# Kernel tuning notes

Hardware: AMD Instinct MI355X
Metric: run time of the kernel (lower is better)

## Reference

```python
import jax, jax.numpy as jnp
import numpy as np

B, L, D_IN, H = 16, 2048, 1024, 512  # bidirectional: out_size = 2*H = D_IN (k=3 SRU layout)


def setup_inputs() -> dict:
    key = jax.random.key(0)
    k1, k2, k3, k4 = jax.random.split(key, 4)
    x = jax.random.normal(k1, (B, L, D_IN), dtype=jnp.float32)
    W = jax.random.normal(k2, (D_IN, 2, H, 3), dtype=jnp.float32) * 0.02
    bf = jax.random.normal(k3, (2, H), dtype=jnp.float32) * 0.02
    br = jax.random.normal(k4, (2, H), dtype=jnp.float32) * 0.02
    return {"x": x, "W": W, "bf": bf, "br": br}


def _sru_scan(xtil, f, r, xres, reverse):
    # xtil/f/r/xres: (L, B, H). Diagonal linear recurrence:
    #   c_t = f_t * c_{t-1} + (1 - f_t) * xtil_t
    #   h_t = r_t * tanh(c_t) + (1 - r_t) * xres_t
    def step(c, inp):
        xt_, f_, r_, xr_ = inp
        c = f_ * c + (1.0 - f_) * xt_
        h = r_ * jnp.tanh(c) + (1.0 - r_) * xr_
        return c, h
    c0 = jnp.zeros(xtil.shape[1:], dtype=xtil.dtype)
    c_last, h = jax.lax.scan(step, c0, (xtil, f, r, xres), reverse=reverse)
    return h, c_last


def reference(x, W, bf, br):
    xt = jnp.transpose(x, (1, 0, 2))  # (L, B, D_IN), as the wrapper does x.transpose(0,1)
    # U: (L, B, 2 dirs, H, 3 = [x_tilde, f_pre, r_pre])
    U = jnp.einsum("lbi,idhk->lbdhk", xt, W)
    f = jax.nn.sigmoid(U[..., 1] + bf[None, None, :, :])  # (L,B,2,H)
    r = jax.nn.sigmoid(U[..., 2] + br[None, None, :, :])
    xtil = U[..., 0]
    # highway/residual: raw input split per direction since n_in == 2*H (k=3)
    xres = xt.reshape(L, B, 2, H)

    h_f, c_f = _sru_scan(xtil[:, :, 0], f[:, :, 0], r[:, :, 0], xres[:, :, 0], reverse=False)
    h_b, c_b = _sru_scan(xtil[:, :, 1], f[:, :, 1], r[:, :, 1], xres[:, :, 1], reverse=True)

    h = jnp.concatenate([h_f, h_b], axis=-1)          # (L, B, 2H)
    c = jnp.concatenate([c_f, c_b], axis=-1)          # (B, 2H) final cell states
    # wrapper returns (out.transpose(0,1), c.transpose(0,1))
    return jnp.transpose(h, (1, 0, 2)), c.T
```

## Files before the change

kernel.cpp:

```cpp
#include <hip/hip_runtime.h>
#include <stdint.h>

#define B_    16
#define L_    2048
#define DIN_  1024
#define H_    512
#define NCOL_ 3072
#define M_    (B_ * L_)
#define K_    DIN_
#define NCHUNK 16
#define CHUNK  128

typedef unsigned short u16;
typedef __bf16 bf16_t;
typedef bf16_t bf16x8 __attribute__((ext_vector_type(8)));
typedef float  f32x4  __attribute__((ext_vector_type(4)));

__device__ __forceinline__ u16 f2bf(float f) {
  union { float f; uint32_t u; } v; v.f = f;
  return (u16)((v.u + 0x7fffu + ((v.u >> 16) & 1u)) >> 16);
}
__device__ __forceinline__ float bf2f(u16 b) {
  union { uint32_t u; float f; } v; v.u = ((uint32_t)b) << 16; return v.f;
}
__device__ __forceinline__ u16 f2h(float f) {
  _Float16 h = (_Float16)f; return *(u16*)&h;
}
__device__ __forceinline__ float h2f(u16 b) {
  _Float16 h = *(_Float16*)&b; return (float)h;
}

__global__ void cvt_x_kernel(const float4* __restrict__ x, ushort4* __restrict__ xb) {
  int i = blockIdx.x * blockDim.x + threadIdx.x;
  float4 v = x[i];
  ushort4 o;
  o.x = f2bf(v.x); o.y = f2bf(v.y); o.z = f2bf(v.z); o.w = f2bf(v.w);
  xb[i] = o;
}

__global__ void transpose_w_kernel(const float* __restrict__ W, u16* __restrict__ Wt) {
  __shared__ float s[32][33];
  int n0 = blockIdx.x * 32;
  int i0 = blockIdx.y * 32;
  int tx = threadIdx.x, ty = threadIdx.y;
  #pragma unroll
  for (int y = 0; y < 32; y += 8)
    s[ty + y][tx] = W[(uint64_t)(i0 + ty + y) * NCOL_ + n0 + tx];
  __syncthreads();
  #pragma unroll
  for (int y = 0; y < 32; y += 8) {
    int n = n0 + ty + y;
    int kk = n % 3, d = n / 1536, h = (n % 1536) / 3;
    int np = kk * 1024 + d * 512 + h;
    Wt[(uint64_t)np * K_ + i0 + tx] = f2bf(s[tx][ty + y]);
  }
}

__device__ __forceinline__ void gload_lds16(const void* g, void* lds) {
  __builtin_amdgcn_global_load_lds(
      (const __attribute__((address_space(1))) uint32_t*)g,
      (__attribute__((address_space(3))) uint32_t*)lds, 16, 0, 0);
}

__device__ __forceinline__ bf16x8 lds_rd(const u16* lds, int byteOff) {
  return __builtin_bit_cast(bf16x8, *(const f32x4*)((const char*)lds + byteOff));
}

__global__ __launch_bounds__(512, 2) void gemm_u_kernel(const u16* __restrict__ A,
                                                        const u16* __restrict__ Bt,
                                                        const float* __restrict__ bfp,
                                                        const float* __restrict__ brp,
                                                        u16* __restrict__ xtilP,
                                                        u16* __restrict__ fP,
                                                        u16* __restrict__ rP) {
  __shared__ __align__(16) u16 lds[81920];

  const int bid = blockIdx.x;
  const int xcd = bid & 7;
  const int li  = bid >> 3;
  const int bm  = xcd * 16 + (li & 15);
  const int bn  = li >> 4;
  const int m0 = bm * 256, n0 = bn * 256;

  const int tid  = threadIdx.x;
  const int w    = tid >> 6, lane = tid & 63;
  const int wr   = w >> 2, wc = w & 3;
  const int rr   = lane & 15, hs = lane >> 4;
  const int swzRd = (rr & 7) << 4;
  const int hsOff = hs * 16;

  const int rStage = w * 8 + (lane >> 3);
  const int sCol   = ((lane & 7) ^ ((lane >> 3) & 7)) * 8;
  const int ldsChunk = w * 1024;

  f32x4 acc[8][4] = {};

  auto stageA = [&](int bufBase, int kt) {
    #pragma unroll
    for (int h = 0; h < 2; ++h)
      #pragma unroll
      for (int j = 0; j < 2; ++j)
        gload_lds16(A + (uint64_t)(m0 + h * 128 + j * 64 + rStage) * K_ + kt + sCol,
                    (char*)lds + bufBase + h * 16384 + j * 8192 + ldsChunk);
  };
  auto stageB = [&](int bufBase, int kt) {
    #pragma unroll
    for (int h = 0; h < 2; ++h)
      #pragma unroll
      for (int j = 0; j < 2; ++j)
        gload_lds16(Bt + (uint64_t)(n0 + h * 128 + j * 64 + rStage) * K_ + kt + sCol,
                    (char*)lds + bufBase + h * 16384 + j * 8192 + ldsChunk);
  };

  stageA(0, 0);
  stageB(65536, 0);
  stageB(65536 + 32768, 64);
  asm volatile("s_waitcnt vmcnt(4)" ::: "memory");
  __builtin_amdgcn_sched_barrier(0);
  __builtin_amdgcn_s_barrier();

  const int aHalfBase = wr * 16384;
  const int bQuart    = (wc >> 1) * 16384;
  const int rowB0     = (wc & 1) * 64;

  int b3 = 0;
  for (int t = 0; t < 16; ++t) {
    const int curA = (t & 1) << 15;
    const int curB = 65536 + b3 * 32768;
    const int b3n2 = (b3 >= 1) ? (b3 - 1) : 2;

    if (t < 15) stageA((~t & 1) << 15, (t + 1) * 64);
    bf16x8 aF[4][2], bF[4][2];
    #pragma unroll
    for (int a = 0; a < 4; ++a)
      #pragma unroll
      for (int ks = 0; ks < 2; ++ks)
        aF[a][ks] = lds_rd(lds, curA + aHalfBase + (a * 16 + rr) * 128 + ((ks * 64 + hsOff) ^ swzRd));
    #pragma unroll
    for (int ni = 0; ni < 4; ++ni)
      #pragma unroll
      for (int ks = 0; ks < 2; ++ks)
        bF[ni][ks] = lds_rd(lds, curB + bQuart + (rowB0 + ni * 16 + rr) * 128 + ((ks * 64 + hsOff) ^ swzRd));
    __builtin_amdgcn_sched_barrier(0);
    __builtin_amdgcn_s_barrier();
    asm volatile("s_waitcnt lgkmcnt(0)" ::: "memory");
    __builtin_amdgcn_sched_barrier(0);
    __builtin_amdgcn_s_setprio(1);
    #pragma unroll
    for (int a = 0; a < 4; ++a)
      #pragma unroll
      for (int ni = 0; ni < 4; ++ni)
        #pragma unroll
        for (int ks = 0; ks < 2; ++ks)
          acc[a][ni] = __builtin_amdgcn_mfma_f32_16x16x32_bf16(aF[a][ks], bF[ni][ks], acc[a][ni], 0, 0, 0);
    __builtin_amdgcn_s_setprio(0);
    __builtin_amdgcn_sched_barrier(0);
    __builtin_amdgcn_s_barrier();

    if (t < 14) stageB(65536 + b3n2 * 32768, (t + 2) * 64);
    bf16x8 aG[4][2];
    #pragma unroll
    for (int a = 0; a < 4; ++a)
      #pragma unroll
      for (int ks = 0; ks < 2; ++ks)
        aG[a][ks] = lds_rd(lds, curA + aHalfBase + ((a + 4) * 16 + rr) * 128 + ((ks * 64 + hsOff) ^ swzRd));
    __builtin_amdgcn_sched_barrier(0);
    __builtin_amdgcn_s_barrier();
    asm volatile("s_waitcnt lgkmcnt(0)" ::: "memory");
    __builtin_amdgcn_sched_barrier(0);
    __builtin_amdgcn_s_setprio(1);
    #pragma unroll
    for (int a = 0; a < 4; ++a)
      #pragma unroll
      for (int ni = 0; ni < 4; ++ni)
        #pragma unroll
        for (int ks = 0; ks < 2; ++ks)
          acc[a + 4][ni] = __builtin_amdgcn_mfma_f32_16x16x32_bf16(aG[a][ks], bF[ni][ks], acc[a + 4][ni], 0, 0, 0);
    __builtin_amdgcn_s_setprio(0);
    if (t < 14) {
      asm volatile("s_waitcnt vmcnt(4)" ::: "memory");
      __builtin_amdgcn_sched_barrier(0);
    } else if (t == 14) {
      asm volatile("s_waitcnt vmcnt(0)" ::: "memory");
      __builtin_amdgcn_sched_barrier(0);
    }
    __builtin_amdgcn_s_barrier();

    b3 = (b3 + 1 == 3) ? 0 : b3 + 1;
  }

  const int kkPlane = n0 >> 10;
  const int chBase  = n0 & 1023;
  u16* plane = (kkPlane == 0) ? xtilP : (kkPlane == 1 ? fP : rP);
  const float* biasp = (kkPlane == 1) ? bfp : brp;
  #pragma unroll
  for (int mi = 0; mi < 8; ++mi) {
    #pragma unroll
    for (int ni = 0; ni < 4; ++ni) {
      const int ch = chBase + wc * 64 + ni * 16 + rr;
      const float bias = kkPlane ? biasp[ch] : 0.f;
      #pragma unroll
      for (int i = 0; i < 4; ++i) {
        const int row = m0 + wr * 128 + mi * 16 + hs * 4 + i;
        float v = acc[mi][ni][i];
        if (kkPlane) v = 1.f / (1.f + __expf(-(v + bias)));
        plane[(uint64_t)row * 1024 + ch] = f2h(v);
      }
    }
  }
}

__global__ __launch_bounds__(256) void scan_partial_kernel(const u16* __restrict__ xtilP,
                                                           const u16* __restrict__ fP,
                                                           float* __restrict__ cpart,
                                                           float* __restrict__ Pp) {
  int tid = blockIdx.x * 256 + threadIdx.x;
  int ch = tid & 1023, chunk = (tid >> 10) & (NCHUNK - 1), b = tid >> 14;
  int d = ch >> 9;
  int l = chunk * CHUNK + (d ? CHUNK - 1 : 0);
  int64_t stride = d ? -1024 : 1024;
  uint64_t base = ((uint64_t)b * L_ + l) * 1024 + ch;
  float c = 0.f, P = 1.f;
  #pragma unroll 4
  for (int it = 0; it < CHUNK; ++it) {
    float f  = h2f(fP[base]);
    float xt = h2f(xtilP[base]);
    c = f * c + (1.f - f) * xt;
    P *= f;
    base += stride;
  }
  int o = (b * NCHUNK + chunk) * 1024 + ch;
  cpart[o] = c;
  Pp[o] = P;
}

__global__ void scan_combine_kernel(const float* __restrict__ cpart, const float* __restrict__ Pp,
                                    float* __restrict__ cin, float* __restrict__ outc) {
  int tid = blockIdx.x * blockDim.x + threadIdx.x;
  int ch = tid & 1023, b = tid >> 10, d = ch >> 9;
  float c = 0.f;
  for (int i = 0; i < NCHUNK; ++i) {
    int chunk = d ? (NCHUNK - 1 - i) : i;
    int o = (b * NCHUNK + chunk) * 1024 + ch;
    cin[o] = c;
    c = cpart[o] + Pp[o] * c;
  }
  outc[ch * B_ + b] = c;
}

__global__ __launch_bounds__(256) void scan_final_kernel(const u16* __restrict__ xb,
                                                         const u16* __restrict__ xtilP,
                                                         const u16* __restrict__ fP,
                                                         const u16* __restrict__ rP,
                                                         const float* __restrict__ cin,
                                                         float* __restrict__ outh) {
  int tid = blockIdx.x * 256 + threadIdx.x;
  int ch = tid & 1023, chunk = (tid >> 10) & (NCHUNK - 1), b = tid >> 14;
  int d = ch >> 9;
  int l = chunk * CHUNK + (d ? CHUNK - 1 : 0);
  int64_t stride = d ? -1024 : 1024;
  uint64_t base = ((uint64_t)b * L_ + l) * 1024 + ch;
  float c = cin[(b * NCHUNK + chunk) * 1024 + ch];
  #pragma unroll 2
  for (int it = 0; it < CHUNK; ++it) {
    float f    = h2f(fP[base]);
    float xt   = h2f(xtilP[base]);
    float rr   = h2f(rP[base]);
    float xres = bf2f(xb[base]);
    c = f * c + (1.f - f) * xt;
    float th = 1.f - 2.f / (__expf(2.f * c) + 1.f);
    outh[base] = rr * th + (1.f - rr) * xres;
    base += stride;
  }
}

extern "C" void kernel_launch(void* const* d_in, const int* in_sizes, int n_in,
                              void* d_out, int out_size, void* d_ws, size_t ws_size,
                              hipStream_t stream) {
  const float* x   = (const float*)d_in[0];
  const float* W   = (const float*)d_in[1];
  const float* bfp = (const float*)d_in[2];
  const float* brp = (const float*)d_in[3];

  float* outh = (float*)d_out;
  float* outc = outh + (size_t)B_ * L_ * DIN_;

  u16* xb = (u16*)d_ws;
  u16* Wt = xb + (size_t)M_ * K_;
  u16* xtilP = Wt + (size_t)NCOL_ * K_;
  u16* fP    = xtilP + (size_t)M_ * 1024;
  u16* rP    = fP    + (size_t)M_ * 1024;
  float* cpart = (float*)Wt;
  float* Pp    = cpart + (size_t)B_ * NCHUNK * 1024;
  float* cin   = Pp    + (size_t)B_ * NCHUNK * 1024;

  cvt_x_kernel<<<(M_ * K_ / 4) / 256, 256, 0, stream>>>((const float4*)x, (ushort4*)xb);
  transpose_w_kernel<<<dim3(NCOL_ / 32, K_ / 32), dim3(32, 8), 0, stream>>>(W, Wt);
  gemm_u_kernel<<<(M_ / 256) * (NCOL_ / 256), 512, 0, stream>>>(xb, Wt, bfp, brp, xtilP, fP, rP);
  scan_partial_kernel<<<(B_ * NCHUNK * 1024) / 256, 256, 0, stream>>>(xtilP, fP, cpart, Pp);
  scan_combine_kernel<<<(B_ * 2 * H_) / 256, 256, 0, stream>>>(cpart, Pp, cin, outc);
  scan_final_kernel<<<(B_ * NCHUNK * 1024) / 256, 256, 0, stream>>>(xb, xtilP, fP, rP, cin, outh);
}
```

Baseline: 384.6 us.

## Collapse GEMM k-loop to single barrier and interleave A fragment loads with MFMAs

The main GEMM loop drops its two mid-iteration barriers and explicit lgkmcnt waits, issuing both the A and B global-to-LDS stages at the top of each iteration. A-fragment reads are split into four pairs of row blocks, each interleaved with its MFMAs, so LDS reads can overlap matrix math and fewer registers are live at once. The loop is marked unroll 1, and the final iteration skips its trailing barrier. The aim is less synchronization and better overlap, but the code relies on the compiler's own waitcnt placement and loses the setprio hints. Safety rests on the existing triple-buffered B and double-buffered A schedule.

```diff
diff --git a/kernel.cpp b/kernel.cpp
--- a/kernel.cpp
+++ b/kernel.cpp
@@ -124,59 +124,39 @@
   const int rowB0     = (wc & 1) * 64;
 
   int b3 = 0;
+  #pragma unroll 1
   for (int t = 0; t < 16; ++t) {
     const int curA = (t & 1) << 15;
     const int curB = 65536 + b3 * 32768;
     const int b3n2 = (b3 >= 1) ? (b3 - 1) : 2;
 
     if (t < 15) stageA((~t & 1) << 15, (t + 1) * 64);
-    bf16x8 aF[4][2], bF[4][2];
-    #pragma unroll
-    for (int a = 0; a < 4; ++a)
-      #pragma unroll
-      for (int ks = 0; ks < 2; ++ks)
-        aF[a][ks] = lds_rd(lds, curA + aHalfBase + (a * 16 + rr) * 128 + ((ks * 64 + hsOff) ^ swzRd));
+    if (t < 14) stageB(65536 + b3n2 * 32768, (t + 2) * 64);
+
+    bf16x8 bF[4][2];
     #pragma unroll
     for (int ni = 0; ni < 4; ++ni)
       #pragma unroll
       for (int ks = 0; ks < 2; ++ks)
         bF[ni][ks] = lds_rd(lds, curB + bQuart + (rowB0 + ni * 16 + rr) * 128 + ((ks * 64 + hsOff) ^ swzRd));
-    __builtin_amdgcn_sched_barrier(0);
-    __builtin_amdgcn_s_barrier();
-    asm volatile("s_waitcnt lgkmcnt(0)" ::: "memory");
-    __builtin_amdgcn_sched_barrier(0);
-    __builtin_amdgcn_s_setprio(1);
-    #pragma unroll
-    for (int a = 0; a < 4; ++a)
+
+    #pragma unroll
+    for (int q = 0; q < 4; ++q) {
+      bf16x8 a0[2], a1[2];
+      #pragma unroll
+      for (int ks = 0; ks < 2; ++ks) {
+        a0[ks] = lds_rd(lds, curA + aHalfBase + ((2 * q) * 16 + rr) * 128 + ((ks * 64 + hsOff) ^ swzRd));
+        a1[ks] = lds_rd(lds, curA + aHalfBase + ((2 * q + 1) * 16 + rr) * 128 + ((ks * 64 + hsOff) ^ swzRd));
+      }
       #pragma unroll
       for (int ni = 0; ni < 4; ++ni)
         #pragma unroll
-        for (int ks = 0; ks < 2; ++ks)
-          acc[a][ni] = __builtin_amdgcn_mfma_f32_16x16x32_bf16(aF[a][ks], bF[ni][ks], acc[a][ni], 0, 0, 0);
-    __builtin_amdgcn_s_setprio(0);
-    __builtin_amdgcn_sched_barrier(0);
-    __builtin_amdgcn_s_barrier();
-
-    if (t < 14) stageB(65536 + b3n2 * 32768, (t + 2) * 64);
-    bf16x8 aG[4][2];
-    #pragma unroll
-    for (int a = 0; a < 4; ++a)
-      #pragma unroll
-      for (int ks = 0; ks < 2; ++ks)
-        aG[a][ks] = lds_rd(lds, curA + aHalfBase + ((a + 4) * 16 + rr) * 128 + ((ks * 64 + hsOff) ^ swzRd));
-    __builtin_amdgcn_sched_barrier(0);
-    __builtin_amdgcn_s_barrier();
-    asm volatile("s_waitcnt lgkmcnt(0)" ::: "memory");
-    __builtin_amdgcn_sched_barrier(0);
-    __builtin_amdgcn_s_setprio(1);
-    #pragma unroll
-    for (int a = 0; a < 4; ++a)
-      #pragma unroll
-      for (int ni = 0; ni < 4; ++ni)
-        #pragma unroll
-        for (int ks = 0; ks < 2; ++ks)
-          acc[a + 4][ni] = __builtin_amdgcn_mfma_f32_16x16x32_bf16(aG[a][ks], bF[ni][ks], acc[a + 4][ni], 0, 0, 0);
-    __builtin_amdgcn_s_setprio(0);
+        for (int ks = 0; ks < 2; ++ks) {
+          acc[2 * q][ni]     = __builtin_amdgcn_mfma_f32_16x16x32_bf16(a0[ks], bF[ni][ks], acc[2 * q][ni], 0, 0, 0);
+          acc[2 * q + 1][ni] = __builtin_amdgcn_mfma_f32_16x16x32_bf16(a1[ks], bF[ni][ks], acc[2 * q + 1][ni], 0, 0, 0);
+        }
+    }
+
     if (t < 14) {
       asm volatile("s_waitcnt vmcnt(4)" ::: "memory");
       __builtin_amdgcn_sched_barrier(0);
@@ -184,7 +164,7 @@
       asm volatile("s_waitcnt vmcnt(0)" ::: "memory");
       __builtin_amdgcn_sched_barrier(0);
     }
-    __builtin_amdgcn_s_barrier();
+    if (t < 15) __builtin_amdgcn_s_barrier();
 
     b3 = (b3 + 1 == 3) ? 0 : b3 + 1;
   }
```

Measured after the change: 381.0 us, median of 2. No clear change (-0.9%).
